# Kernel tuning notes

Measured on AMD Instinct MI355X. Metric: run time of the kernel, lower is better.

Reference implementation:

```python
import jax, jax.numpy as jnp
import numpy as np
from jax.ops import segment_sum

N_NODES = 100000


def _graph_conv(feats, W, b, prelu_a, src, dst):
    """DGL GraphConv with norm='both' + PReLU activation.
    feats: [N, Din], W: [Din, Dout], src/dst: [E] int32.
    """
    ones = jnp.ones(src.shape, feats.dtype)
    deg_out = segment_sum(ones, src, num_segments=N_NODES)  # out-degree of src nodes
    deg_in = segment_sum(ones, dst, num_segments=N_NODES)   # in-degree of dst nodes
    norm_s = jnp.where(deg_out > 0, jax.lax.rsqrt(jnp.maximum(deg_out, 1.0)), 0.0)
    norm_d = jnp.where(deg_in > 0, jax.lax.rsqrt(jnp.maximum(deg_in, 1.0)), 0.0)
    x = feats * norm_s[:, None]                      # [N, Din]
    agg = segment_sum(x[src], dst, num_segments=N_NODES)  # SpMM: [N, Din]
    agg = agg * norm_d[:, None]
    h = agg @ W + b                                   # [N, Dout]
    # PReLU with single shared slope
    return jnp.where(h > 0, h, prelu_a * h)


def setup_inputs() -> dict:
    key = jax.random.key(0)
    ks = jax.random.split(key, 7)
    N, Din, Dout, E = N_NODES, 128, 128, 800000
    feats = jax.random.normal(ks[0], (N, Din), jnp.float32)
    W = jax.random.normal(ks[1], (Din, Dout), jnp.float32) * (1.0 / np.sqrt(Din))
    b = jnp.zeros((Dout,), jnp.float32)
    prelu_a = jnp.full((1,), 0.25, jnp.float32)
    src_pos = jax.random.randint(ks[2], (E,), 0, N, jnp.int32)
    dst_pos = jax.random.randint(ks[3], (E,), 0, N, jnp.int32)
    src_neg = jax.random.randint(ks[4], (E,), 0, N, jnp.int32)
    dst_neg = jax.random.randint(ks[5], (E,), 0, N, jnp.int32)
    return {"feats": feats, "W": W, "b": b, "prelu_a": prelu_a,
            "src_pos": src_pos, "dst_pos": dst_pos,
            "src_neg": src_neg, "dst_neg": dst_neg}


def reference(feats, W, b, prelu_a, src_pos, dst_pos, src_neg, dst_neg):
    h_pos = _graph_conv(feats, W, b, prelu_a, src_pos, dst_pos)
    h_neg = _graph_conv(feats, W, b, prelu_a, src_neg, dst_neg)
    return jnp.stack([h_pos, h_neg])  # [2, N, Dout]
```

## Files before the change

### kernel.cpp

```cpp
#include <hip/hip_runtime.h>

#define NN 100000
#define DD 128
#define NB ((NN + 255) / 256)

__global__ __launch_bounds__(256) void count_kernel(
    const int* __restrict__ sp, const int* __restrict__ dp,
    const int* __restrict__ sn, const int* __restrict__ dn,
    int* __restrict__ icnt, int E) {
  int i = blockIdx.x * 256 + threadIdx.x;
  if (i < E) {
    atomicAdd(&icnt[sp[i]], 1);
    atomicAdd(&icnt[NN + dp[i]], 1);
    atomicAdd(&icnt[2 * NN + sn[i]], 1);
    atomicAdd(&icnt[3 * NN + dn[i]], 1);
  }
}

__global__ __launch_bounds__(256) void norm_kernel(
    const int* __restrict__ icnt, float* __restrict__ norm, int n) {
  int i = blockIdx.x * 256 + threadIdx.x;
  if (i < n) {
    int c = icnt[i];
    norm[i] = (c > 0) ? rsqrtf((float)c) : 0.0f;
  }
}

__global__ __launch_bounds__(256) void scan_p1(
    const int* __restrict__ icnt, int* __restrict__ part) {
  const int* cnt = icnt + (blockIdx.y == 0 ? NN : 3 * NN);
  __shared__ int sdata[256];
  int i = blockIdx.x * 256 + threadIdx.x;
  sdata[threadIdx.x] = (i < NN) ? cnt[i] : 0;
  __syncthreads();
  for (int off = 128; off > 0; off >>= 1) {
    if (threadIdx.x < off) sdata[threadIdx.x] += sdata[threadIdx.x + off];
    __syncthreads();
  }
  if (threadIdx.x == 0) part[blockIdx.y * NB + blockIdx.x] = sdata[0];
}

__global__ __launch_bounds__(64) void scan_p2(int* __restrict__ part,
                                              int* __restrict__ rs_p,
                                              int* __restrict__ rs_n, int E) {
  int t = threadIdx.x;
  if (t < 2) {
    int* p = part + t * NB;
    int run = 0;
    for (int i = 0; i < NB; ++i) {
      int v = p[i];
      p[i] = run;
      run += v;
    }
    int* rs = t == 0 ? rs_p : rs_n;
    rs[NN] = E;
  }
}

__global__ __launch_bounds__(256) void scan_p3(
    const int* __restrict__ icnt, const int* __restrict__ part,
    int* __restrict__ rs_p, int* __restrict__ rs_n, int* __restrict__ cur) {
  int set = blockIdx.y;
  const int* cnt = icnt + (set == 0 ? NN : 3 * NN);
  int* rs = set == 0 ? rs_p : rs_n;
  int* cu = cur + set * NN;
  __shared__ int sdata[256];
  int t = threadIdx.x;
  int i = blockIdx.x * 256 + t;
  int v = (i < NN) ? cnt[i] : 0;
  sdata[t] = v;
  __syncthreads();
  for (int off = 1; off < 256; off <<= 1) {
    int x = (t >= off) ? sdata[t - off] : 0;
    __syncthreads();
    sdata[t] += x;
    __syncthreads();
  }
  if (i < NN) {
    int start = part[set * NB + blockIdx.x] + sdata[t] - v;
    rs[i] = start;
    cu[i] = start;
  }
}

__global__ __launch_bounds__(256) void fill_kernel(
    const int* __restrict__ sp, const int* __restrict__ dp,
    const int* __restrict__ sn, const int* __restrict__ dn,
    int* __restrict__ cur, int* __restrict__ es_p, int* __restrict__ es_n,
    int E) {
  int i = blockIdx.x * 256 + threadIdx.x;
  if (i < E) {
    int p = atomicAdd(&cur[dp[i]], 1);
    es_p[p] = sp[i];
    int q = atomicAdd(&cur[NN + dn[i]], 1);
    es_n[q] = sn[i];
  }
}

__device__ __forceinline__ float f4c(const float4 v, int k) {
  return k == 0 ? v.x : (k == 1 ? v.y : (k == 2 ? v.z : v.w));
}

__global__ __launch_bounds__(256) void gemm128_kernel(
    const float* __restrict__ A, const float* __restrict__ W,
    float* __restrict__ Y, int nrows) {
  __shared__ float Ws[128 * 128];
  int t = threadIdx.x;
  {
    const float4* W4 = (const float4*)W;
    float4* Ws4 = (float4*)Ws;
#pragma unroll
    for (int j = 0; j < 16; ++j) {
      int i = t + 256 * j;
      Ws4[i] = W4[i];
    }
  }
  __syncthreads();

  int tx = t & 15, ty = t >> 4;
  int row0 = blockIdx.x * 64;
  const float4* A4 = (const float4*)A;
  const float4* Ws4 = (const float4*)Ws;

  float acc[4][8];
#pragma unroll
  for (int i = 0; i < 4; ++i)
#pragma unroll
    for (int j = 0; j < 8; ++j) acc[i][j] = 0.0f;

  int r[4];
  bool valid[4];
#pragma unroll
  for (int i = 0; i < 4; ++i) {
    r[i] = row0 + ty * 4 + i;
    valid[i] = r[i] < nrows;
  }

  for (int kc = 0; kc < 32; ++kc) {
    float4 a4[4];
#pragma unroll
    for (int i = 0; i < 4; ++i) {
      a4[i] = valid[i] ? A4[(size_t)r[i] * 32 + kc]
                       : make_float4(0.f, 0.f, 0.f, 0.f);
    }
#pragma unroll
    for (int kk = 0; kk < 4; ++kk) {
      int k = kc * 4 + kk;
      float4 w0 = Ws4[k * 32 + tx];
      float4 w1 = Ws4[k * 32 + 16 + tx];
      float wv[8] = {w0.x, w0.y, w0.z, w0.w, w1.x, w1.y, w1.z, w1.w};
#pragma unroll
      for (int i = 0; i < 4; ++i) {
        float av = f4c(a4[i], kk);
#pragma unroll
        for (int j = 0; j < 8; ++j) acc[i][j] += av * wv[j];
      }
    }
  }

  float4* Y4 = (float4*)Y;
#pragma unroll
  for (int i = 0; i < 4; ++i) {
    if (valid[i]) {
      float4 o0 = {acc[i][0], acc[i][1], acc[i][2], acc[i][3]};
      float4 o1 = {acc[i][4], acc[i][5], acc[i][6], acc[i][7]};
      Y4[(size_t)r[i] * 32 + tx] = o0;
      Y4[(size_t)r[i] * 32 + 16 + tx] = o1;
    }
  }
}

__global__ __launch_bounds__(256) void gather_finalize_kernel(
    const float4* __restrict__ y4, const int* __restrict__ rs_p,
    const int* __restrict__ rs_n, const int* __restrict__ es_p,
    const int* __restrict__ es_n, const float* __restrict__ norm,
    const float* __restrict__ b, const float* __restrict__ prelu_a,
    float4* __restrict__ out4) {
  int idx = blockIdx.x * 256 + threadIdx.x;
  int lane = idx & 31;
  int R = idx >> 5;
  if (R >= 2 * NN) return;
  int set = R >= NN;
  int r = R - set * NN;

  const int* rs = set ? rs_n : rs_p;
  const int* es = set ? es_n : es_p;
  const float* ns = norm + (set ? 2 * NN : 0);
  const float* ndv = norm + (set ? 3 * NN : NN);

  int j0 = rs[r], j1 = rs[r + 1];
  float4 acc = make_float4(0.f, 0.f, 0.f, 0.f);
  for (int j = j0; j < j1; ++j) {
    int s = es[j];
    float sc = ns[s];
    float4 v = y4[(size_t)s * 32 + lane];
    acc.x += sc * v.x;
    acc.y += sc * v.y;
    acc.z += sc * v.z;
    acc.w += sc * v.w;
  }
  float nd = ndv[r];
  float a = prelu_a[0];
  float4 bb = ((const float4*)b)[lane];
  float4 h;
  h.x = acc.x * nd + bb.x;
  h.y = acc.y * nd + bb.y;
  h.z = acc.z * nd + bb.z;
  h.w = acc.w * nd + bb.w;
  h.x = h.x > 0.f ? h.x : a * h.x;
  h.y = h.y > 0.f ? h.y : a * h.y;
  h.z = h.z > 0.f ? h.z : a * h.z;
  h.w = h.w > 0.f ? h.w : a * h.w;
  out4[(size_t)R * 32 + lane] = h;
}

extern "C" void kernel_launch(void* const* d_in, const int* in_sizes, int n_in,
                              void* d_out, int out_size, void* d_ws, size_t ws_size,
                              hipStream_t stream) {
  const float* feats = (const float*)d_in[0];
  const float* W = (const float*)d_in[1];
  const float* b = (const float*)d_in[2];
  const float* pa = (const float*)d_in[3];
  const int* sp = (const int*)d_in[4];
  const int* dp = (const int*)d_in[5];
  const int* sn = (const int*)d_in[6];
  const int* dn = (const int*)d_in[7];
  int E = in_sizes[4];

  float* y = (float*)d_ws;
  float* norm = y + (size_t)NN * DD;
  int* icnt = (int*)(norm + 4 * NN);
  int* rs_p = icnt + 4 * NN;
  int* rs_n = rs_p + NN + 1;
  int* cur = rs_n + NN + 1;
  int* es_p = cur + 2 * NN;
  int* es_n = es_p + E;
  int* part = es_n + E;

  hipMemsetAsync(icnt, 0, (size_t)4 * NN * sizeof(int), stream);

  count_kernel<<<(E + 255) / 256, 256, 0, stream>>>(sp, dp, sn, dn, icnt, E);
  norm_kernel<<<(4 * NN + 255) / 256, 256, 0, stream>>>(icnt, norm, 4 * NN);

  dim3 g1(NB, 2);
  scan_p1<<<g1, 256, 0, stream>>>(icnt, part);
  scan_p2<<<1, 64, 0, stream>>>(part, rs_p, rs_n, E);
  scan_p3<<<g1, 256, 0, stream>>>(icnt, part, rs_p, rs_n, cur);

  fill_kernel<<<(E + 255) / 256, 256, 0, stream>>>(sp, dp, sn, dn, cur, es_p,
                                                   es_n, E);

  gemm128_kernel<<<(NN + 63) / 64, 256, 0, stream>>>(feats, W, y, NN);

  gather_finalize_kernel<<<(2 * NN * 32 + 255) / 256, 256, 0, stream>>>(
      (const float4*)y, rs_p, rs_n, es_p, es_n, norm, b, pa, (float4*)d_out);
}
```

Baseline: 649.3 us.

## Use split-bf16 MFMA GEMM, parallelize block-offset scan, nontemporal edge stores

Replaces the fp32 FMA GEMM with an MFMA 16x16x32 bf16 kernel that keeps near-fp32 accuracy. Each operand is split into a hi and a lo bf16 part, and three products are accumulated per tile. A small prep kernel lays W out in fragment order, reusing the cursor workspace region once the fill step is done with it. The single-thread serial scan over block partial sums becomes a 512-thread shared-memory scan, removing a long serial latency chain. Edge-list writes in the fill step use nontemporal stores to reduce cache pollution.

```diff
diff --git a/kernel.cpp b/kernel.cpp
--- a/kernel.cpp
+++ b/kernel.cpp
@@ -1,8 +1,22 @@
 #include <hip/hip_runtime.h>
+#include <stdint.h>
 
 #define NN 100000
 #define DD 128
 #define NB ((NN + 255) / 256)
+
+typedef short bf16x8 __attribute__((ext_vector_type(8)));
+typedef float f32x4 __attribute__((ext_vector_type(4)));
+
+__device__ __forceinline__ unsigned short f2bf(float f) {
+  unsigned int x = __builtin_bit_cast(unsigned int, f);
+  unsigned int r = x + 0x7fffu + ((x >> 16) & 1u);
+  return (unsigned short)(r >> 16);
+}
+__device__ __forceinline__ float bf2f(unsigned short b) {
+  unsigned int x = ((unsigned int)b) << 16;
+  return __builtin_bit_cast(float, x);
+}
 
 __global__ __launch_bounds__(256) void count_kernel(
     const int* __restrict__ sp, const int* __restrict__ dp,
@@ -40,20 +54,28 @@
   if (threadIdx.x == 0) part[blockIdx.y * NB + blockIdx.x] = sdata[0];
 }
 
-__global__ __launch_bounds__(64) void scan_p2(int* __restrict__ part,
-                                              int* __restrict__ rs_p,
-                                              int* __restrict__ rs_n, int E) {
+__global__ __launch_bounds__(512) void scan_p2(int* __restrict__ part,
+                                               int* __restrict__ rs_p,
+                                               int* __restrict__ rs_n, int E) {
+  __shared__ int s[512];
   int t = threadIdx.x;
-  if (t < 2) {
-    int* p = part + t * NB;
-    int run = 0;
-    for (int i = 0; i < NB; ++i) {
-      int v = p[i];
-      p[i] = run;
-      run += v;
-    }
-    int* rs = t == 0 ? rs_p : rs_n;
-    rs[NN] = E;
+#pragma unroll
+  for (int set = 0; set < 2; ++set) {
+    int v = (t < NB) ? part[set * NB + t] : 0;
+    s[t] = v;
+    __syncthreads();
+    for (int off = 1; off < 512; off <<= 1) {
+      int x = (t >= off) ? s[t - off] : 0;
+      __syncthreads();
+      s[t] += x;
+      __syncthreads();
+    }
+    if (t < NB) part[set * NB + t] = s[t] - v;
+    __syncthreads();
+  }
+  if (t == 0) {
+    rs_p[NN] = E;
+    rs_n[NN] = E;
   }
 }
 
@@ -91,81 +113,82 @@
   int i = blockIdx.x * 256 + threadIdx.x;
   if (i < E) {
     int p = atomicAdd(&cur[dp[i]], 1);
-    es_p[p] = sp[i];
+    __builtin_nontemporal_store(sp[i], es_p + p);
     int q = atomicAdd(&cur[NN + dn[i]], 1);
-    es_n[q] = sn[i];
-  }
-}
-
-__device__ __forceinline__ float f4c(const float4 v, int k) {
-  return k == 0 ? v.x : (k == 1 ? v.y : (k == 2 ? v.z : v.w));
-}
-
-__global__ __launch_bounds__(256) void gemm128_kernel(
-    const float* __restrict__ A, const float* __restrict__ W,
-    float* __restrict__ Y, int nrows) {
-  __shared__ float Ws[128 * 128];
-  int t = threadIdx.x;
-  {
-    const float4* W4 = (const float4*)W;
-    float4* Ws4 = (float4*)Ws;
-#pragma unroll
-    for (int j = 0; j < 16; ++j) {
-      int i = t + 256 * j;
-      Ws4[i] = W4[i];
-    }
-  }
-  __syncthreads();
-
-  int tx = t & 15, ty = t >> 4;
-  int row0 = blockIdx.x * 64;
-  const float4* A4 = (const float4*)A;
-  const float4* Ws4 = (const float4*)Ws;
-
-  float acc[4][8];
-#pragma unroll
-  for (int i = 0; i < 4; ++i)
-#pragma unroll
-    for (int j = 0; j < 8; ++j) acc[i][j] = 0.0f;
-
-  int r[4];
-  bool valid[4];
-#pragma unroll
-  for (int i = 0; i < 4; ++i) {
-    r[i] = row0 + ty * 4 + i;
-    valid[i] = r[i] < nrows;
-  }
-
-  for (int kc = 0; kc < 32; ++kc) {
-    float4 a4[4];
-#pragma unroll
-    for (int i = 0; i < 4; ++i) {
-      a4[i] = valid[i] ? A4[(size_t)r[i] * 32 + kc]
-                       : make_float4(0.f, 0.f, 0.f, 0.f);
-    }
-#pragma unroll
-    for (int kk = 0; kk < 4; ++kk) {
-      int k = kc * 4 + kk;
-      float4 w0 = Ws4[k * 32 + tx];
-      float4 w1 = Ws4[k * 32 + 16 + tx];
-      float wv[8] = {w0.x, w0.y, w0.z, w0.w, w1.x, w1.y, w1.z, w1.w};
-#pragma unroll
-      for (int i = 0; i < 4; ++i) {
-        float av = f4c(a4[i], kk);
-#pragma unroll
-        for (int j = 0; j < 8; ++j) acc[i][j] += av * wv[j];
-      }
-    }
-  }
-
-  float4* Y4 = (float4*)Y;
-#pragma unroll
-  for (int i = 0; i < 4; ++i) {
-    if (valid[i]) {
-      float4 o0 = {acc[i][0], acc[i][1], acc[i][2], acc[i][3]};
-      float4 o1 = {acc[i][4], acc[i][5], acc[i][6], acc[i][7]};
-      Y4[(size_t)r[i] * 32 + tx] = o0;
-      Y4[(size_t)r[i] * 32 + 16 + tx] = o1;
+    __builtin_nontemporal_store(sn[i], es_n + q);
+  }
+}
+
+__global__ __launch_bounds__(256) void wprep_kernel(
+    const float* __restrict__ W, unsigned short* __restrict__ Wf_hi,
+    unsigned short* __restrict__ Wf_lo) {
+  int idx = blockIdx.x * 256 + threadIdx.x;
+  int c = idx >> 11;
+  int t = (idx >> 9) & 3;
+  int l = (idx >> 3) & 63;
+  int j = idx & 7;
+  int k = t * 32 + ((l >> 4) << 3) + j;
+  int n = c * 16 + (l & 15);
+  float w = W[k * 128 + n];
+  unsigned short hi = f2bf(w);
+  float lo = w - bf2f(hi);
+  Wf_hi[idx] = hi;
+  Wf_lo[idx] = f2bf(lo);
+}
+
+__global__ __launch_bounds__(256) void gemm_mfma_kernel(
+    const float* __restrict__ A, const unsigned short* __restrict__ Wf_hi,
+    const unsigned short* __restrict__ Wf_lo, float* __restrict__ Y,
+    int nrows) {
+  int wave = threadIdx.x >> 6;
+  int lane = threadIdx.x & 63;
+  int r0 = blockIdx.x * 64 + wave * 16;
+  int arow = r0 + (lane & 15);
+  int kg = lane >> 4;
+
+  f32x4 acc[8];
+#pragma unroll
+  for (int c = 0; c < 8; ++c) acc[c] = (f32x4)(0.0f);
+
+  bool avalid = arow < nrows;
+  const float* abase = A + (size_t)arow * 128 + kg * 8;
+
+#pragma unroll
+  for (int t = 0; t < 4; ++t) {
+    float av[8];
+    if (avalid) {
+      float4 a0 = ((const float4*)(abase + t * 32))[0];
+      float4 a1 = ((const float4*)(abase + t * 32))[1];
+      av[0] = a0.x; av[1] = a0.y; av[2] = a0.z; av[3] = a0.w;
+      av[4] = a1.x; av[5] = a1.y; av[6] = a1.z; av[7] = a1.w;
+    } else {
+#pragma unroll
+      for (int j = 0; j < 8; ++j) av[j] = 0.0f;
+    }
+    union { bf16x8 v; unsigned short u[8]; } ah, al;
+#pragma unroll
+    for (int j = 0; j < 8; ++j) {
+      unsigned short h = f2bf(av[j]);
+      ah.u[j] = h;
+      al.u[j] = f2bf(av[j] - bf2f(h));
+    }
+#pragma unroll
+    for (int c = 0; c < 8; ++c) {
+      const bf16x8 bh = *(const bf16x8*)(Wf_hi + (((c * 4 + t) * 64 + lane) << 3));
+      const bf16x8 bl = *(const bf16x8*)(Wf_lo + (((c * 4 + t) * 64 + lane) << 3));
+      acc[c] = __builtin_amdgcn_mfma_f32_16x16x32_bf16(ah.v, bh, acc[c], 0, 0, 0);
+      acc[c] = __builtin_amdgcn_mfma_f32_16x16x32_bf16(al.v, bh, acc[c], 0, 0, 0);
+      acc[c] = __builtin_amdgcn_mfma_f32_16x16x32_bf16(ah.v, bl, acc[c], 0, 0, 0);
+    }
+  }
+
+#pragma unroll
+  for (int j = 0; j < 4; ++j) {
+    int orow = r0 + kg * 4 + j;
+    if (orow < nrows) {
+      float* yr = Y + (size_t)orow * 128 + (lane & 15);
+#pragma unroll
+      for (int c = 0; c < 8; ++c) yr[c * 16] = acc[c][j];
     }
   }
 }
@@ -236,6 +259,9 @@
   int* es_p = cur + 2 * NN;
   int* es_n = es_p + E;
   int* part = es_n + E;
+  unsigned short* Wf_hi =
+      (unsigned short*)(((uintptr_t)cur + 15) & ~(uintptr_t)15);
+  unsigned short* Wf_lo = Wf_hi + 16384;
 
   hipMemsetAsync(icnt, 0, (size_t)4 * NN * sizeof(int), stream);
 
@@ -244,13 +270,15 @@
 
   dim3 g1(NB, 2);
   scan_p1<<<g1, 256, 0, stream>>>(icnt, part);
-  scan_p2<<<1, 64, 0, stream>>>(part, rs_p, rs_n, E);
+  scan_p2<<<1, 512, 0, stream>>>(part, rs_p, rs_n, E);
   scan_p3<<<g1, 256, 0, stream>>>(icnt, part, rs_p, rs_n, cur);
 
   fill_kernel<<<(E + 255) / 256, 256, 0, stream>>>(sp, dp, sn, dn, cur, es_p,
                                                    es_n, E);
 
-  gemm128_kernel<<<(NN + 63) / 64, 256, 0, stream>>>(feats, W, y, NN);
+  wprep_kernel<<<64, 256, 0, stream>>>(W, Wf_hi, Wf_lo);
+  gemm_mfma_kernel<<<(NN + 63) / 64, 256, 0, stream>>>(feats, Wf_hi, Wf_lo, y,
+                                                       NN);
 
   gather_finalize_kernel<<<(2 * NN * 32 + 255) / 256, 256, 0, stream>>>(
       (const float4*)y, rs_p, rs_n, es_p, es_n, norm, b, pa, (float4*)d_out);
```

After: 573.4 us. -11.7%, faster.
